# Performance work log

Hardware: AMD Instinct MI355X
Metric: run time of the kernel (lower is better)

The kernel has to match this reference:

```python
import jax, jax.numpy as jnp
import numpy as np

NEG_INF = -jnp.inf


def apply_top_k_top_p(logits, k, p):
    """Faithful port of vllm apply_top_k_top_p (both k and p given).
    logits: [B, V] float; k: [B] int (1..V); p: [B] float in (0,1].
    """
    B, V = logits.shape
    # ascending sort, as in torch logits.sort(descending=False)
    idx = jnp.argsort(logits, axis=-1)                      # [B, V]
    ls = jnp.take_along_axis(logits, idx, axis=-1)          # [B, V] sorted ascending
    # ---- top-k: threshold = k-th largest = sorted[V - k] ----
    thr_idx = (V - k.astype(jnp.int32))[:, None]            # [B, 1]
    thr = jnp.take_along_axis(ls, thr_idx, axis=-1)         # [B, 1]
    ls = jnp.where(ls < thr, NEG_INF, ls)
    # ---- top-p: mask smallest tail whose cumulative prob <= 1 - p ----
    probs_sort = jax.nn.softmax(ls, axis=-1)
    probs_sum = jnp.cumsum(probs_sort, axis=-1)
    top_p_mask = probs_sum <= (1.0 - p)[:, None]
    # last (largest) element is never masked
    col = jnp.arange(V)
    top_p_mask = top_p_mask & (col[None, :] != V - 1)
    ls = jnp.where(top_p_mask, NEG_INF, ls)
    # ---- scatter back to original positions ----
    rows = jnp.arange(B)[:, None]
    return jnp.zeros_like(logits).at[rows, idx].set(ls)


def setup_inputs() -> dict:
    key = jax.random.key(0)
    k1, k2, k3, k4 = jax.random.split(key, 4)
    B, V = 256, 128000
    logits = jax.random.normal(k1, (B, V), dtype=jnp.float32) * 4.0
    k = jax.random.randint(k2, (B,), 1, V + 1, dtype=jnp.int32)
    p = jax.random.uniform(k3, (B,), dtype=jnp.float32, minval=0.05, maxval=1.0)
    # Exp(1) noise, replacing torch q.exponential_() in random_sample
    q = jax.random.exponential(k4, (B, V), dtype=jnp.float32)
    return {"logits": logits, "k": k, "p": p, "q": q}


def reference(logits, k, p, q):
    masked = apply_top_k_top_p(logits, k, p)
    # logprobs_mode == 'processed_logprobs'
    logprobs = jax.nn.log_softmax(masked.astype(jnp.float32), axis=-1)
    probs = jax.nn.softmax(masked.astype(jnp.float32), axis=-1)
    # random_sample: argmax(probs / Exp(1) noise) == Gumbel-max style sampling
    next_token_ids = jnp.argmax(probs / q, axis=-1).reshape(-1)
    return next_token_ids, logprobs
```

## Files before the change

kernel.cpp:

```cpp
#include <hip/hip_runtime.h>
#include <stdint.h>
#include <math.h>

#define TPB 1024
#define NWAVE 16
#define NBINS 8192
#define CAP 4096
#define TIE_CAP 4096
#define NEG_SENTINEL -1.0e30f

struct Scal {
  double Eacc, T, T2, Zall, D, Zf, logZf, Wtmp, Wb1b, cumexcl;
  float M;
  int b1, bw, m;
  unsigned int trank, sel, ccur, cnt_tmp;
  unsigned int n1, n2, cnt_v, ntie, cnt_b1;
};

__device__ __forceinline__ unsigned int f2key(float x) {
  unsigned int b = __float_as_uint(x);
  return (b & 0x80000000u) ? ~b : (b | 0x80000000u);
}
__device__ __forceinline__ float key2f(unsigned int u) {
  unsigned int b = (u & 0x80000000u) ? (u ^ 0x80000000u) : ~u;
  return __uint_as_float(b);
}

__global__ __launch_bounds__(TPB, 1) void topk_topp_kernel(
    const float* __restrict__ logits, const int* __restrict__ kk,
    const float* __restrict__ pp, const float* __restrict__ qq,
    float* __restrict__ out, int B, int V)
{
  __shared__ __align__(16) char smem[123392];
  double* w_hist = (double*)smem;
  double* col_w  = (double*)smem;
  unsigned int* cnt_hist = (unsigned int*)(smem + 65536);
  unsigned int* col_key  = (unsigned int*)(smem + 65536);
  unsigned int* col_idx  = (unsigned int*)(smem + 81920);
  unsigned int* b1_keys  = (unsigned int*)(smem + 98304);
  unsigned int* tie_idx  = (unsigned int*)(smem + 98304);
  double* dscan = (double*)(smem + 114688);
  unsigned int* uscan = (unsigned int*)(smem + 114688);
  float* fscan = (float*)(smem + 114688);
  Scal* S = (Scal*)(smem + 122880);

  const int row = blockIdx.x;
  const int tid = threadIdx.x;
  const size_t roff = (size_t)row * (size_t)V;
  const float* L = logits + roff;
  const float* Q = qq + roff;
  float* OLP = out + B + roff;
  const int V4 = V >> 2;
  const float4* L4 = (const float4*)L;
  const float4* Q4 = (const float4*)Q;

  for (int i = tid; i < NBINS; i += TPB) cnt_hist[i] = 0u;
  if (tid == 0) { S->n1 = 0u; S->n2 = 0u; S->cnt_v = 0u; S->ntie = 0u; S->bw = -1; }
  __syncthreads();

  float lmax = -INFINITY;
  for (int j = tid; j < V4; j += TPB) {
    float4 v = L4[j];
    lmax = fmaxf(lmax, fmaxf(fmaxf(v.x, v.y), fmaxf(v.z, v.w)));
    atomicAdd(&cnt_hist[f2key(v.x) >> 19], 1u);
    atomicAdd(&cnt_hist[f2key(v.y) >> 19], 1u);
    atomicAdd(&cnt_hist[f2key(v.z) >> 19], 1u);
    atomicAdd(&cnt_hist[f2key(v.w) >> 19], 1u);
  }
  for (int i = (V4 << 2) + tid; i < V; i += TPB) {
    float x = L[i]; lmax = fmaxf(lmax, x);
    atomicAdd(&cnt_hist[f2key(x) >> 19], 1u);
  }
  #pragma unroll
  for (int o = 32; o; o >>= 1) lmax = fmaxf(lmax, __shfl_down(lmax, o, 64));
  if ((tid & 63) == 0) fscan[tid >> 6] = lmax;
  __syncthreads();
  if (tid == 0) {
    float m = fscan[0];
    for (int i = 1; i < NWAVE; ++i) m = fmaxf(m, fscan[i]);
    S->M = m;
  }
  __syncthreads();
  const float Mf = S->M;
  const double Md = (double)Mf;

  {
    int kv = kk[row]; if (kv < 1) kv = 1; if (kv > V) kv = V;
    unsigned int target = (unsigned int)(V - kv);
    const int per = NBINS / TPB;
    const int base = tid * per;
    unsigned int own = 0;
    for (int b = 0; b < per; ++b) own += cnt_hist[base + b];
    uscan[tid] = own;
    __syncthreads();
    for (int off = 1; off < TPB; off <<= 1) {
      unsigned int v = uscan[tid];
      unsigned int a = (tid >= off) ? uscan[tid - off] : 0u;
      __syncthreads();
      uscan[tid] = v + a;
      __syncthreads();
    }
    unsigned int cum = uscan[tid] - own;
    for (int b = 0; b < per; ++b) {
      unsigned int c = cnt_hist[base + b];
      if (target >= cum && target < cum + c) {
        S->b1 = base + b; S->trank = target - cum; S->cnt_b1 = c;
      }
      cum += c;
    }
  }
  __syncthreads();
  const int b1 = S->b1;
  const unsigned int cnt_b1 = S->cnt_b1;
  const bool fast1 = (cnt_b1 <= (unsigned int)CAP);

  for (int i = tid; i < NBINS; i += TPB) w_hist[i] = 0.0;
  __syncthreads();
  for (int j = tid; j < V4; j += TPB) {
    float4 v = L4[j];
    float xs[4] = {v.x, v.y, v.z, v.w};
    #pragma unroll
    for (int c = 0; c < 4; ++c) {
      float x = xs[c];
      unsigned int u = f2key(x);
      double e = exp((double)x - Md);
      unsafeAtomicAdd(&w_hist[u >> 19], e);
      if (fast1 && (int)(u >> 19) == b1) {
        unsigned int ppos = atomicAdd(&S->n1, 1u);
        if (ppos < (unsigned int)CAP) b1_keys[ppos] = u;
      }
    }
  }
  for (int i = (V4 << 2) + tid; i < V; i += TPB) {
    float x = L[i];
    unsigned int u = f2key(x);
    double e = exp((double)x - Md);
    unsafeAtomicAdd(&w_hist[u >> 19], e);
    if (fast1 && (int)(u >> 19) == b1) {
      unsigned int ppos = atomicAdd(&S->n1, 1u);
      if (ppos < (unsigned int)CAP) b1_keys[ppos] = u;
    }
  }
  __syncthreads();

  unsigned int thr_key = 0u;
  {
    unsigned int prefix = (unsigned int)b1;
    int plen = 13;
    unsigned int trank = S->trank;
    unsigned int ccur = cnt_b1;
    bool have = fast1;
    while (!have && ccur > (unsigned int)CAP && plen < 32) {
      int nb = 32 - plen; if (nb > 13) nb = 13;
      int nbins = 1 << nb;
      for (int i = tid; i < nbins; i += TPB) cnt_hist[i] = 0u;
      __syncthreads();
      const int shp = 32 - plen, shs = 32 - plen - nb;
      for (int i2 = tid; i2 < V; i2 += TPB) {
        unsigned int u = f2key(L[i2]);
        if ((u >> shp) == prefix) atomicAdd(&cnt_hist[(u >> shs) & (unsigned int)(nbins - 1)], 1u);
      }
      __syncthreads();
      if (tid == 0) {
        unsigned int cum = 0;
        for (int c = 0; c < nbins; ++c) {
          unsigned int cc = cnt_hist[c];
          if (trank >= cum && trank < cum + cc) { S->sel = (unsigned int)c; S->trank = trank - cum; S->ccur = cc; break; }
          cum += cc;
        }
      }
      __syncthreads();
      prefix = (prefix << nb) | S->sel;
      trank = S->trank;
      ccur = S->ccur;
      plen += nb;
    }
    if (!have && ccur <= (unsigned int)CAP) {
      if (tid == 0) S->n1 = 0u;
      __syncthreads();
      const int shp = 32 - plen;
      for (int i2 = tid; i2 < V; i2 += TPB) {
        unsigned int u = f2key(L[i2]);
        if ((u >> shp) == prefix) { unsigned int ppos = atomicAdd(&S->n1, 1u); if (ppos < (unsigned int)CAP) b1_keys[ppos] = u; }
      }
      __syncthreads();
      have = true;
    }
    if (!have) {
      thr_key = prefix;
    } else {
      unsigned int n1e = S->n1; if (n1e > (unsigned int)CAP) n1e = CAP;
      unsigned int lo = prefix << (32 - plen);
      for (int bit = 32 - plen - 1; bit >= 0; --bit) {
        unsigned int mid = lo | (1u << bit);
        unsigned int lc = 0;
        for (unsigned int i2 = tid; i2 < n1e; i2 += TPB) {
          unsigned int u = b1_keys[i2];
          lc += (u >= lo && u < mid) ? 1u : 0u;
        }
        #pragma unroll
        for (int o = 32; o; o >>= 1) lc += __shfl_down(lc, o, 64);
        if ((tid & 63) == 0) uscan[tid >> 6] = lc;
        __syncthreads();
        if (tid == 0) { unsigned int s = 0; for (int i3 = 0; i3 < NWAVE; ++i3) s += uscan[i3]; S->cnt_tmp = s; }
        __syncthreads();
        unsigned int c = S->cnt_tmp;
        if (trank >= c) { trank -= c; lo = mid; }
        __syncthreads();
      }
      thr_key = lo;
    }
  }

  {
    double wl = 0.0;
    if (fast1) {
      unsigned int n1e = S->n1; if (n1e > (unsigned int)CAP) n1e = CAP;
      for (unsigned int i2 = tid; i2 < n1e; i2 += TPB) {
        unsigned int u = b1_keys[i2];
        if (u < thr_key) wl += exp((double)key2f(u) - Md);
      }
    } else {
      for (int i2 = tid; i2 < V; i2 += TPB) {
        float x = L[i2];
        unsigned int u = f2key(x);
        if ((int)(u >> 19) == b1 && u < thr_key) wl += exp((double)x - Md);
      }
    }
    #pragma unroll
    for (int o = 32; o; o >>= 1) wl += __shfl_down(wl, o, 64);
    if ((tid & 63) == 0) dscan[tid >> 6] = wl;
    __syncthreads();
    if (tid == 0) { double s = 0; for (int i3 = 0; i3 < NWAVE; ++i3) s += dscan[i3]; S->Wb1b = s; }
    __syncthreads();
  }
  {
    double za = 0.0, zb = 0.0;
    for (int i = tid; i < NBINS; i += TPB) {
      double w = w_hist[i];
      za += w; if (i < b1) zb += w;
    }
    #pragma unroll
    for (int o = 32; o; o >>= 1) { za += __shfl_down(za, o, 64); zb += __shfl_down(zb, o, 64); }
    if ((tid & 63) == 0) { dscan[tid >> 6] = za; dscan[NWAVE + (tid >> 6)] = zb; }
    __syncthreads();
    if (tid == 0) {
      double sza = 0, szb = 0;
      for (int i3 = 0; i3 < NWAVE; ++i3) { sza += dscan[i3]; szb += dscan[NWAVE + i3]; }
      double D = szb + S->Wb1b;
      S->Zall = sza; S->D = D;
      float pv = pp[row];
      float omp = 1.0f - pv;
      double T = (double)omp * (sza - D);
      S->T = T; S->T2 = T + D;
    }
    __syncthreads();
  }
  {
    const double T2 = S->T2;
    const int per = NBINS / TPB;
    const int base = tid * per;
    double own = 0.0;
    for (int b = 0; b < per; ++b) own += w_hist[base + b];
    dscan[tid] = own;
    __syncthreads();
    for (int off = 1; off < TPB; off <<= 1) {
      double v = dscan[tid];
      double a = (tid >= off) ? dscan[tid - off] : 0.0;
      __syncthreads();
      dscan[tid] = v + a;
      __syncthreads();
    }
    double cum = dscan[tid] - own;
    for (int b = 0; b < per; ++b) {
      double w = w_hist[base + b];
      if (T2 >= cum && T2 < cum + w) { S->bw = base + b; S->cumexcl = cum; }
      cum += w;
    }
    __syncthreads();
    if (tid == 0) {
      if (S->bw < 0) {
        for (int bq = NBINS - 1; bq >= 0; --bq)
          if (w_hist[bq] > 0.0) { S->bw = bq; S->cumexcl = S->Zall - w_hist[bq]; break; }
      }
      double ea = S->cumexcl - S->D;
      S->Eacc = ea > 0.0 ? ea : 0.0;
    }
    __syncthreads();
  }

  unsigned int vstar = 0u; double E_before = 0.0;
  {
    int plen2 = 13;
    unsigned int prefix2 = (unsigned int)S->bw;
    bool direct = false;
    while (true) {
      if (tid == 0) S->n2 = 0u;
      __syncthreads();
      const int shp = 32 - plen2;
      for (int j = tid; j < V4; j += TPB) {
        float4 v = L4[j];
        const int i0 = j << 2;
        float xs[4] = {v.x, v.y, v.z, v.w};
        #pragma unroll
        for (int c = 0; c < 4; ++c) {
          float x = xs[c];
          unsigned int u = f2key(x);
          if (u >= thr_key && (u >> shp) == prefix2) {
            unsigned int ppos = atomicAdd(&S->n2, 1u);
            if (ppos < (unsigned int)CAP) { col_key[ppos] = u; col_idx[ppos] = (unsigned int)(i0 + c); col_w[ppos] = exp((double)x - Md); }
          }
        }
      }
      for (int i2 = (V4 << 2) + tid; i2 < V; i2 += TPB) {
        float x = L[i2]; unsigned int u = f2key(x);
        if (u >= thr_key && (u >> shp) == prefix2) {
          unsigned int ppos = atomicAdd(&S->n2, 1u);
          if (ppos < (unsigned int)CAP) { col_key[ppos] = u; col_idx[ppos] = (unsigned int)i2; col_w[ppos] = exp((double)x - Md); }
        }
      }
      __syncthreads();
      if (S->n2 <= (unsigned int)CAP) break;
      if (plen2 >= 32) { direct = true; break; }
      int nb = 32 - plen2; if (nb > 13) nb = 13;
      int nbins = 1 << nb;
      for (int i = tid; i < nbins; i += TPB) w_hist[i] = 0.0;
      __syncthreads();
      const int shs = 32 - plen2 - nb;
      for (int i2 = tid; i2 < V; i2 += TPB) {
        float x = L[i2]; unsigned int u = f2key(x);
        if (u >= thr_key && (u >> shp) == prefix2)
          unsafeAtomicAdd(&w_hist[(u >> shs) & (unsigned int)(nbins - 1)], exp((double)x - Md));
      }
      __syncthreads();
      if (tid == 0) {
        double Trem = S->T - S->Eacc;
        double cum = 0.0; int csel = -1; double cumsel = 0.0;
        for (int c = 0; c < nbins; ++c) {
          double w = w_hist[c];
          if (Trem >= cum && Trem < cum + w) { csel = c; cumsel = cum; break; }
          cum += w;
        }
        if (csel < 0) {
          cum = 0.0;
          for (int c = 0; c < nbins; ++c) { double w = w_hist[c]; if (w > 0.0) { csel = c; cumsel = cum; } cum += w; }
        }
        S->sel = (unsigned int)csel;
        S->Eacc += cumsel;
      }
      __syncthreads();
      prefix2 = (prefix2 << nb) | S->sel;
      plen2 += nb;
    }

    if (direct) {
      vstar = prefix2; E_before = S->Eacc;
      unsigned int n2e = S->n2; if (n2e > (unsigned int)CAP) n2e = CAP;
      if (n2e > (unsigned int)TIE_CAP) n2e = TIE_CAP;
      for (unsigned int i2 = tid; i2 < n2e; i2 += TPB) tie_idx[i2] = col_idx[i2];
      if (tid == 0) { S->cnt_v = S->n2; S->ntie = n2e; }
      __syncthreads();
    } else {
      unsigned int n2e = S->n2; if (n2e > (unsigned int)CAP) n2e = CAP;
      unsigned int lo = prefix2 << (32 - plen2);
      double Ea = S->Eacc;
      const double T = S->T;
      for (int bit = 32 - plen2 - 1; bit >= 0; --bit) {
        unsigned int mid = lo | (1u << bit);
        double lw = 0.0;
        for (unsigned int i2 = tid; i2 < n2e; i2 += TPB) {
          unsigned int u = col_key[i2];
          if (u >= lo && u < mid) lw += col_w[i2];
        }
        #pragma unroll
        for (int o = 32; o; o >>= 1) lw += __shfl_down(lw, o, 64);
        if ((tid & 63) == 0) dscan[tid >> 6] = lw;
        __syncthreads();
        if (tid == 0) { double s = 0; for (int i3 = 0; i3 < NWAVE; ++i3) s += dscan[i3]; S->Wtmp = s; }
        __syncthreads();
        double W = S->Wtmp;
        if (Ea + W > T) {  } else { Ea += W; lo = mid; }
        __syncthreads();
      }
      vstar = lo; E_before = Ea;
      for (unsigned int i2 = tid; i2 < n2e; i2 += TPB) {
        if (col_key[i2] == vstar) {
          atomicAdd(&S->cnt_v, 1u);
          unsigned int tp = atomicAdd(&S->ntie, 1u);
          if (tp < (unsigned int)TIE_CAP) tie_idx[tp] = col_idx[i2];
        }
      }
      __syncthreads();
    }
  }

  if (tid == 0) {
    double e_v = exp((double)key2f(vstar) - Md);
    double md = floor((S->T - E_before) / e_v);
    double cv = (double)S->cnt_v;
    if (!(md > 0.0)) md = 0.0;
    if (md > cv) md = cv;
    S->m = (int)md;
    double Zk = S->Zall - S->D;
    double Zf = Zk - (E_before + md * e_v);
    if (!(Zf > 1e-300)) Zf = 1e-300;
    S->Zf = Zf; S->logZf = log(Zf);
  }
  __syncthreads();

  const unsigned int vs = vstar;
  const int mth = S->m;
  int nt = (int)S->ntie; if (nt > TIE_CAP) nt = TIE_CAP;
  const float Zff = (float)S->Zf;
  const double lZf = S->logZf;
  float br = -1.0f; int bi = 0x7FFFFFFF;

  for (int j = tid; j < V4; j += TPB) {
    float4 lv = L4[j];
    float4 qv = Q4[j];
    const int i0 = j << 2;
    float xs[4] = {lv.x, lv.y, lv.z, lv.w};
    float qs[4] = {qv.x, qv.y, qv.z, qv.w};
    #pragma unroll
    for (int c = 0; c < 4; ++c) {
      const int i = i0 + c;
      float x = xs[c];
      unsigned int u = f2key(x);
      bool keep;
      if (u > vs) keep = true;
      else if (u == vs) {
        int rk = 0;
        for (int t2 = 0; t2 < nt; ++t2) rk += (tie_idx[t2] < (unsigned int)i) ? 1 : 0;
        keep = (rk >= mth);
      } else keep = false;
      float lp, r;
      if (keep) {
        lp = (float)(((double)x - Md) - lZf);
        float pr = expf(x - Mf) / Zff;
        r = pr / qs[c];
      } else { lp = NEG_SENTINEL; r = 0.0f; }
      OLP[i] = lp;
      if (r > br || (r == br && i < bi)) { br = r; bi = i; }
    }
  }
  for (int i = (V4 << 2) + tid; i < V; i += TPB) {
    float x = L[i];
    unsigned int u = f2key(x);
    bool keep;
    if (u > vs) keep = true;
    else if (u == vs) {
      int rk = 0;
      for (int t2 = 0; t2 < nt; ++t2) rk += (tie_idx[t2] < (unsigned int)i) ? 1 : 0;
      keep = (rk >= mth);
    } else keep = false;
    float lp, r;
    if (keep) {
      lp = (float)(((double)x - Md) - lZf);
      float pr = expf(x - Mf) / Zff;
      r = pr / Q[i];
    } else { lp = NEG_SENTINEL; r = 0.0f; }
    OLP[i] = lp;
    if (r > br || (r == br && i < bi)) { br = r; bi = i; }
  }

  #pragma unroll
  for (int o = 32; o; o >>= 1) {
    float orr = __shfl_down(br, o, 64);
    int oi = __shfl_down(bi, o, 64);
    if (orr > br || (orr == br && oi < bi)) { br = orr; bi = oi; }
  }
  __syncthreads();
  if ((tid & 63) == 0) { fscan[tid >> 6] = br; ((int*)(fscan + NWAVE))[tid >> 6] = bi; }
  __syncthreads();
  if (tid == 0) {
    float bb = fscan[0]; int bbi = ((int*)(fscan + NWAVE))[0];
    for (int i = 1; i < NWAVE; ++i) {
      float r2 = fscan[i]; int ii = ((int*)(fscan + NWAVE))[i];
      if (r2 > bb || (r2 == bb && ii < bbi)) { bb = r2; bbi = ii; }
    }
    out[row] = (float)bbi;
  }
}

extern "C" void kernel_launch(void* const* d_in, const int* in_sizes, int n_in,
                              void* d_out, int out_size, void* d_ws, size_t ws_size,
                              hipStream_t stream) {
  const float* logits = (const float*)d_in[0];
  const int* k = (const int*)d_in[1];
  const float* p = (const float*)d_in[2];
  const float* q = (const float*)d_in[3];
  float* out = (float*)d_out;
  const int B = in_sizes[1];
  const int V = in_sizes[0] / B;
  hipLaunchKernelGGL(topk_topp_kernel, dim3(B), dim3(TPB), 0, stream,
                     logits, k, p, q, out, B, V);
}
```

Baseline: 454.7 us.

## Fuse weight histogram into first pass and replace bit-by-bit radix refinement

```diff
diff --git a/kernel.cpp b/kernel.cpp
--- a/kernel.cpp
+++ b/kernel.cpp
@@ -10,10 +10,10 @@
 #define NEG_SENTINEL -1.0e30f
 
 struct Scal {
-  double Eacc, T, T2, Zall, D, Zf, logZf, Wtmp, Wb1b, cumexcl;
+  double Eacc, T, T2, Zall, D, Zf, logZf, Wb1b, cumexcl;
   float M;
   int b1, bw, m;
-  unsigned int trank, sel, ccur, cnt_tmp;
+  unsigned int trank, sel, ccur;
   unsigned int n1, n2, cnt_v, ntie, cnt_b1;
 };
 
@@ -31,7 +31,7 @@
     const float* __restrict__ pp, const float* __restrict__ qq,
     float* __restrict__ out, int B, int V)
 {
-  __shared__ __align__(16) char smem[123392];
+  __shared__ __align__(16) char smem[118400];
   double* w_hist = (double*)smem;
   double* col_w  = (double*)smem;
   unsigned int* cnt_hist = (unsigned int*)(smem + 65536);
@@ -39,13 +39,18 @@
   unsigned int* col_idx  = (unsigned int*)(smem + 81920);
   unsigned int* b1_keys  = (unsigned int*)(smem + 98304);
   unsigned int* tie_idx  = (unsigned int*)(smem + 98304);
-  double* dscan = (double*)(smem + 114688);
-  unsigned int* uscan = (unsigned int*)(smem + 114688);
-  float* fscan = (float*)(smem + 114688);
-  Scal* S = (Scal*)(smem + 122880);
+  unsigned int* rcnt = (unsigned int*)(smem + 114688);
+  double*       rw   = (double*)(smem + 115712);
+  double*       dw   = (double*)(smem + 117760);
+  unsigned int* uw   = (unsigned int*)(smem + 118016);
+  float*        fw   = (float*)(smem + 118080);
+  int*          iw   = (int*)(smem + 118144);
+  Scal* S = (Scal*)(smem + 118208);
 
   const int row = blockIdx.x;
   const int tid = threadIdx.x;
+  const int lane = tid & 63;
+  const int wid = tid >> 6;
   const size_t roff = (size_t)row * (size_t)V;
   const float* L = logits + roff;
   const float* Q = qq + roff;
@@ -54,105 +59,119 @@
   const float4* L4 = (const float4*)L;
   const float4* Q4 = (const float4*)Q;
 
-  for (int i = tid; i < NBINS; i += TPB) cnt_hist[i] = 0u;
+  for (int i = tid; i < NBINS; i += TPB) { cnt_hist[i] = 0u; w_hist[i] = 0.0; }
   if (tid == 0) { S->n1 = 0u; S->n2 = 0u; S->cnt_v = 0u; S->ntie = 0u; S->bw = -1; }
   __syncthreads();
 
   float lmax = -INFINITY;
   for (int j = tid; j < V4; j += TPB) {
     float4 v = L4[j];
-    lmax = fmaxf(lmax, fmaxf(fmaxf(v.x, v.y), fmaxf(v.z, v.w)));
-    atomicAdd(&cnt_hist[f2key(v.x) >> 19], 1u);
-    atomicAdd(&cnt_hist[f2key(v.y) >> 19], 1u);
-    atomicAdd(&cnt_hist[f2key(v.z) >> 19], 1u);
-    atomicAdd(&cnt_hist[f2key(v.w) >> 19], 1u);
+    float xs[4] = {v.x, v.y, v.z, v.w};
+    #pragma unroll
+    for (int c = 0; c < 4; ++c) {
+      float x = xs[c];
+      lmax = fmaxf(lmax, x);
+      unsigned int u = f2key(x);
+      atomicAdd(&cnt_hist[u >> 19], 1u);
+      float bl = key2f(u & 0xFFF80000u);
+      unsafeAtomicAdd(&w_hist[u >> 19], (double)__expf(x - bl));
+    }
   }
   for (int i = (V4 << 2) + tid; i < V; i += TPB) {
-    float x = L[i]; lmax = fmaxf(lmax, x);
-    atomicAdd(&cnt_hist[f2key(x) >> 19], 1u);
+    float x = L[i];
+    lmax = fmaxf(lmax, x);
+    unsigned int u = f2key(x);
+    atomicAdd(&cnt_hist[u >> 19], 1u);
+    float bl = key2f(u & 0xFFF80000u);
+    unsafeAtomicAdd(&w_hist[u >> 19], (double)__expf(x - bl));
   }
   #pragma unroll
   for (int o = 32; o; o >>= 1) lmax = fmaxf(lmax, __shfl_down(lmax, o, 64));
-  if ((tid & 63) == 0) fscan[tid >> 6] = lmax;
+  if (lane == 0) fw[wid] = lmax;
   __syncthreads();
   if (tid == 0) {
-    float m = fscan[0];
-    for (int i = 1; i < NWAVE; ++i) m = fmaxf(m, fscan[i]);
+    float m = fw[0];
+    for (int i = 1; i < NWAVE; ++i) m = fmaxf(m, fw[i]);
     S->M = m;
   }
   __syncthreads();
   const float Mf = S->M;
   const double Md = (double)Mf;
 
+  for (int i = tid; i < NBINS; i += TPB) {
+    double w = w_hist[i];
+    if (w != 0.0) {
+      float bl = key2f(((unsigned int)i) << 19);
+      w_hist[i] = w * exp((double)bl - Md);
+    }
+  }
+  __syncthreads();
+
   {
     int kv = kk[row]; if (kv < 1) kv = 1; if (kv > V) kv = V;
-    unsigned int target = (unsigned int)(V - kv);
-    const int per = NBINS / TPB;
-    const int base = tid * per;
+    const unsigned int target = (unsigned int)(V - kv);
+    const int base = tid * 8;
     unsigned int own = 0;
-    for (int b = 0; b < per; ++b) own += cnt_hist[base + b];
-    uscan[tid] = own;
-    __syncthreads();
-    for (int off = 1; off < TPB; off <<= 1) {
-      unsigned int v = uscan[tid];
-      unsigned int a = (tid >= off) ? uscan[tid - off] : 0u;
-      __syncthreads();
-      uscan[tid] = v + a;
-      __syncthreads();
-    }
-    unsigned int cum = uscan[tid] - own;
-    for (int b = 0; b < per; ++b) {
+    #pragma unroll
+    for (int b = 0; b < 8; ++b) own += cnt_hist[base + b];
+    unsigned int inc = own;
+    #pragma unroll
+    for (int o = 1; o < 64; o <<= 1) {
+      unsigned int t = __shfl_up(inc, (unsigned)o, 64);
+      if (lane >= o) inc += t;
+    }
+    if (lane == 63) uw[wid] = inc;
+    __syncthreads();
+    if (tid == 0) {
+      unsigned int c = 0;
+      for (int w = 0; w < NWAVE; ++w) { unsigned int t = uw[w]; uw[w] = c; c += t; }
+    }
+    __syncthreads();
+    unsigned int cum = uw[wid] + (inc - own);
+    for (int b = 0; b < 8; ++b) {
       unsigned int c = cnt_hist[base + b];
-      if (target >= cum && target < cum + c) {
+      if (c && target >= cum && target < cum + c) {
         S->b1 = base + b; S->trank = target - cum; S->cnt_b1 = c;
       }
       cum += c;
     }
   }
   __syncthreads();
+
   const int b1 = S->b1;
   const unsigned int cnt_b1 = S->cnt_b1;
   const bool fast1 = (cnt_b1 <= (unsigned int)CAP);
-
-  for (int i = tid; i < NBINS; i += TPB) w_hist[i] = 0.0;
-  __syncthreads();
-  for (int j = tid; j < V4; j += TPB) {
-    float4 v = L4[j];
-    float xs[4] = {v.x, v.y, v.z, v.w};
-    #pragma unroll
-    for (int c = 0; c < 4; ++c) {
-      float x = xs[c];
-      unsigned int u = f2key(x);
-      double e = exp((double)x - Md);
-      unsafeAtomicAdd(&w_hist[u >> 19], e);
-      if (fast1 && (int)(u >> 19) == b1) {
-        unsigned int ppos = atomicAdd(&S->n1, 1u);
-        if (ppos < (unsigned int)CAP) b1_keys[ppos] = u;
-      }
-    }
-  }
-  for (int i = (V4 << 2) + tid; i < V; i += TPB) {
-    float x = L[i];
-    unsigned int u = f2key(x);
-    double e = exp((double)x - Md);
-    unsafeAtomicAdd(&w_hist[u >> 19], e);
-    if (fast1 && (int)(u >> 19) == b1) {
-      unsigned int ppos = atomicAdd(&S->n1, 1u);
-      if (ppos < (unsigned int)CAP) b1_keys[ppos] = u;
-    }
-  }
-  __syncthreads();
-
-  unsigned int thr_key = 0u;
-  {
-    unsigned int prefix = (unsigned int)b1;
-    int plen = 13;
-    unsigned int trank = S->trank;
+  const float bl1 = key2f(((unsigned int)b1) << 19);
+  const double fac1 = exp((double)bl1 - Md);
+
+  unsigned int prefix = (unsigned int)b1;
+  int plen = 13;
+  if (fast1) {
+    for (int j = tid; j < V4; j += TPB) {
+      float4 v = L4[j];
+      float xs[4] = {v.x, v.y, v.z, v.w};
+      #pragma unroll
+      for (int c = 0; c < 4; ++c) {
+        unsigned int u = f2key(xs[c]);
+        if ((int)(u >> 19) == b1) {
+          unsigned int pos = atomicAdd(&S->n1, 1u);
+          if (pos < (unsigned int)CAP) b1_keys[pos] = u;
+        }
+      }
+    }
+    for (int i = (V4 << 2) + tid; i < V; i += TPB) {
+      unsigned int u = f2key(L[i]);
+      if ((int)(u >> 19) == b1) {
+        unsigned int pos = atomicAdd(&S->n1, 1u);
+        if (pos < (unsigned int)CAP) b1_keys[pos] = u;
+      }
+    }
+    __syncthreads();
+  } else {
     unsigned int ccur = cnt_b1;
-    bool have = fast1;
-    while (!have && ccur > (unsigned int)CAP && plen < 32) {
+    while (ccur > (unsigned int)CAP && plen < 32) {
       int nb = 32 - plen; if (nb > 13) nb = 13;
-      int nbins = 1 << nb;
+      const int nbins = 1 << nb;
       for (int i = tid; i < nbins; i += TPB) cnt_hist[i] = 0u;
       __syncthreads();
       const int shp = 32 - plen, shs = 32 - plen - nb;
@@ -162,76 +181,85 @@
       }
       __syncthreads();
       if (tid == 0) {
-        unsigned int cum = 0;
+        unsigned int trank = S->trank, cum = 0;
         for (int c = 0; c < nbins; ++c) {
           unsigned int cc = cnt_hist[c];
-          if (trank >= cum && trank < cum + cc) { S->sel = (unsigned int)c; S->trank = trank - cum; S->ccur = cc; break; }
+          if (cc && trank < cum + cc) { S->sel = (unsigned int)c; S->trank = trank - cum; S->ccur = cc; break; }
           cum += cc;
         }
       }
       __syncthreads();
       prefix = (prefix << nb) | S->sel;
-      trank = S->trank;
       ccur = S->ccur;
       plen += nb;
     }
-    if (!have && ccur <= (unsigned int)CAP) {
-      if (tid == 0) S->n1 = 0u;
-      __syncthreads();
-      const int shp = 32 - plen;
-      for (int i2 = tid; i2 < V; i2 += TPB) {
-        unsigned int u = f2key(L[i2]);
-        if ((u >> shp) == prefix) { unsigned int ppos = atomicAdd(&S->n1, 1u); if (ppos < (unsigned int)CAP) b1_keys[ppos] = u; }
-      }
-      __syncthreads();
-      have = true;
-    }
-    if (!have) {
-      thr_key = prefix;
-    } else {
-      unsigned int n1e = S->n1; if (n1e > (unsigned int)CAP) n1e = CAP;
-      unsigned int lo = prefix << (32 - plen);
-      for (int bit = 32 - plen - 1; bit >= 0; --bit) {
-        unsigned int mid = lo | (1u << bit);
-        unsigned int lc = 0;
-        for (unsigned int i2 = tid; i2 < n1e; i2 += TPB) {
-          unsigned int u = b1_keys[i2];
-          lc += (u >= lo && u < mid) ? 1u : 0u;
-        }
-        #pragma unroll
-        for (int o = 32; o; o >>= 1) lc += __shfl_down(lc, o, 64);
-        if ((tid & 63) == 0) uscan[tid >> 6] = lc;
-        __syncthreads();
-        if (tid == 0) { unsigned int s = 0; for (int i3 = 0; i3 < NWAVE; ++i3) s += uscan[i3]; S->cnt_tmp = s; }
-        __syncthreads();
-        unsigned int c = S->cnt_tmp;
-        if (trank >= c) { trank -= c; lo = mid; }
-        __syncthreads();
-      }
-      thr_key = lo;
-    }
-  }
+    if (tid == 0) S->n1 = 0u;
+    __syncthreads();
+    const int shp = 32 - plen;
+    for (int i2 = tid; i2 < V; i2 += TPB) {
+      unsigned int u = f2key(L[i2]);
+      if ((u >> shp) == prefix) {
+        unsigned int pos = atomicAdd(&S->n1, 1u);
+        if (pos < (unsigned int)CAP) b1_keys[pos] = u;
+      }
+    }
+    __syncthreads();
+  }
+
+  {
+    const unsigned int n1e = (S->n1 < (unsigned int)CAP) ? S->n1 : (unsigned int)CAP;
+    while (plen < 32) {
+      int nb = 32 - plen; if (nb > 8) nb = 8;
+      const int shp = 32 - plen, shs = 32 - plen - nb;
+      const unsigned int msk = (1u << nb) - 1u;
+      if (tid < 256) rcnt[tid] = 0u;
+      __syncthreads();
+      for (unsigned int i = tid; i < n1e; i += TPB) {
+        unsigned int u = b1_keys[i];
+        if ((u >> shp) == prefix) atomicAdd(&rcnt[(u >> shs) & msk], 1u);
+      }
+      __syncthreads();
+      if (tid == 0) {
+        unsigned int trank = S->trank, cum = 0; int sel = -1;
+        const int nbn = 1 << nb;
+        for (int c = 0; c < nbn; ++c) {
+          unsigned int cc = rcnt[c];
+          if (cc && trank < cum + cc) { sel = c; S->trank = trank - cum; break; }
+          cum += cc;
+        }
+        if (sel < 0) {
+          for (int c = nbn - 1; c >= 0; --c) if (rcnt[c]) { sel = c; S->trank = rcnt[c] - 1u; break; }
+          if (sel < 0) sel = 0;
+        }
+        S->sel = (unsigned int)sel;
+      }
+      __syncthreads();
+      prefix = (prefix << nb) | S->sel;
+      plen += nb;
+    }
+  }
+  const unsigned int thr_key = prefix;
 
   {
     double wl = 0.0;
     if (fast1) {
-      unsigned int n1e = S->n1; if (n1e > (unsigned int)CAP) n1e = CAP;
-      for (unsigned int i2 = tid; i2 < n1e; i2 += TPB) {
-        unsigned int u = b1_keys[i2];
-        if (u < thr_key) wl += exp((double)key2f(u) - Md);
+      const unsigned int n1e = (S->n1 < (unsigned int)CAP) ? S->n1 : (unsigned int)CAP;
+      for (unsigned int i = tid; i < n1e; i += TPB) {
+        unsigned int u = b1_keys[i];
+        if (u < thr_key) wl += (double)__expf(key2f(u) - bl1);
       }
     } else {
       for (int i2 = tid; i2 < V; i2 += TPB) {
         float x = L[i2];
         unsigned int u = f2key(x);
-        if ((int)(u >> 19) == b1 && u < thr_key) wl += exp((double)x - Md);
+        if ((int)(u >> 19) == b1 && u < thr_key) wl += (double)__expf(x - bl1);
       }
     }
     #pragma unroll
     for (int o = 32; o; o >>= 1) wl += __shfl_down(wl, o, 64);
-    if ((tid & 63) == 0) dscan[tid >> 6] = wl;
-    __syncthreads();
-    if (tid == 0) { double s = 0; for (int i3 = 0; i3 < NWAVE; ++i3) s += dscan[i3]; S->Wb1b = s; }
+    if (lane == 0) dw[wid] = wl;
+    __syncthreads();
+    if (tid == 0) { double s = 0; for (int i = 0; i < NWAVE; ++i) s += dw[i]; S->Wb1b = s * fac1; }
     __syncthreads();
   }
   {
@@ -242,11 +270,11 @@
     }
     #pragma unroll
     for (int o = 32; o; o >>= 1) { za += __shfl_down(za, o, 64); zb += __shfl_down(zb, o, 64); }
-    if ((tid & 63) == 0) { dscan[tid >> 6] = za; dscan[NWAVE + (tid >> 6)] = zb; }
+    if (lane == 0) { dw[wid] = za; dw[NWAVE + wid] = zb; }
     __syncthreads();
     if (tid == 0) {
       double sza = 0, szb = 0;
-      for (int i3 = 0; i3 < NWAVE; ++i3) { sza += dscan[i3]; szb += dscan[NWAVE + i3]; }
+      for (int i = 0; i < NWAVE; ++i) { sza += dw[i]; szb += dw[NWAVE + i]; }
       double D = szb + S->Wb1b;
       S->Zall = sza; S->D = D;
       float pv = pp[row];
@@ -256,25 +284,30 @@
     }
     __syncthreads();
   }
+
   {
     const double T2 = S->T2;
-    const int per = NBINS / TPB;
-    const int base = tid * per;
+    const int base = tid * 8;
     double own = 0.0;
-    for (int b = 0; b < per; ++b) own += w_hist[base + b];
-    dscan[tid] = own;
-    __syncthreads();
-    for (int off = 1; off < TPB; off <<= 1) {
-      double v = dscan[tid];
-      double a = (tid >= off) ? dscan[tid - off] : 0.0;
-      __syncthreads();
-      dscan[tid] = v + a;
-      __syncthreads();
-    }
-    double cum = dscan[tid] - own;
-    for (int b = 0; b < per; ++b) {
+    #pragma unroll
+    for (int b = 0; b < 8; ++b) own += w_hist[base + b];
+    double incd = own;
+    #pragma unroll
+    for (int o = 1; o < 64; o <<= 1) {
+      double t = __shfl_up(incd, (unsigned)o, 64);
+      if (lane >= o) incd += t;
+    }
+    if (lane == 63) dw[wid] = incd;
+    __syncthreads();
+    if (tid == 0) {
+      double c = 0;
+      for (int w = 0; w < NWAVE; ++w) { double t = dw[w]; dw[w] = c; c += t; }
+    }
+    __syncthreads();
+    double cum = dw[wid] + (incd - own);
+    for (int b = 0; b < 8; ++b) {
       double w = w_hist[base + b];
-      if (T2 >= cum && T2 < cum + w) { S->bw = base + b; S->cumexcl = cum; }
+      if (w > 0.0 && T2 >= cum && T2 < cum + w) { S->bw = base + b; S->cumexcl = cum; }
       cum += w;
     }
     __syncthreads();
@@ -291,8 +324,11 @@
 
   unsigned int vstar = 0u; double E_before = 0.0;
   {
+    const int bwv = S->bw;
+    const float blw = key2f(((unsigned int)bwv) << 19);
+    const double facw = exp((double)blw - Md);
     int plen2 = 13;
-    unsigned int prefix2 = (unsigned int)S->bw;
+    unsigned int prefix2 = (unsigned int)bwv;
     bool direct = false;
     while (true) {
       if (tid == 0) S->n2 = 0u;
@@ -307,45 +343,54 @@
           float x = xs[c];
           unsigned int u = f2key(x);
           if (u >= thr_key && (u >> shp) == prefix2) {
-            unsigned int ppos = atomicAdd(&S->n2, 1u);
-            if (ppos < (unsigned int)CAP) { col_key[ppos] = u; col_idx[ppos] = (unsigned int)(i0 + c); col_w[ppos] = exp((double)x - Md); }
+            unsigned int pos = atomicAdd(&S->n2, 1u);
+            if (pos < (unsigned int)CAP) {
+              col_key[pos] = u; col_idx[pos] = (unsigned int)(i0 + c);
+              col_w[pos] = (double)__expf(x - blw) * facw;
+            }
           }
         }
       }
       for (int i2 = (V4 << 2) + tid; i2 < V; i2 += TPB) {
-        float x = L[i2]; unsigned int u = f2key(x);
+        float x = L[i2];
+        unsigned int u = f2key(x);
         if (u >= thr_key && (u >> shp) == prefix2) {
-          unsigned int ppos = atomicAdd(&S->n2, 1u);
-          if (ppos < (unsigned int)CAP) { col_key[ppos] = u; col_idx[ppos] = (unsigned int)i2; col_w[ppos] = exp((double)x - Md); }
+          unsigned int pos = atomicAdd(&S->n2, 1u);
+          if (pos < (unsigned int)CAP) {
+            col_key[pos] = u; col_idx[pos] = (unsigned int)i2;
+            col_w[pos] = (double)__expf(x - blw) * facw;
+          }
         }
       }
       __syncthreads();
       if (S->n2 <= (unsigned int)CAP) break;
       if (plen2 >= 32) { direct = true; break; }
       int nb = 32 - plen2; if (nb > 13) nb = 13;
-      int nbins = 1 << nb;
+      const int nbins = 1 << nb;
       for (int i = tid; i < nbins; i += TPB) w_hist[i] = 0.0;
       __syncthreads();
       const int shs = 32 - plen2 - nb;
       for (int i2 = tid; i2 < V; i2 += TPB) {
-        float x = L[i2]; unsigned int u = f2key(x);
+        float x = L[i2];
+        unsigned int u = f2key(x);
         if (u >= thr_key && (u >> shp) == prefix2)
-          unsafeAtomicAdd(&w_hist[(u >> shs) & (unsigned int)(nbins - 1)], exp((double)x - Md));
+          unsafeAtomicAdd(&w_hist[(u >> shs) & (unsigned int)(nbins - 1)], (double)__expf(x - blw) * facw);
       }
       __syncthreads();
       if (tid == 0) {
         double Trem = S->T - S->Eacc;
-        double cum = 0.0; int csel = -1; double cumsel = 0.0;
+        double cum = 0.0; int sel = -1; double cumsel = 0.0;
         for (int c = 0; c < nbins; ++c) {
           double w = w_hist[c];
-          if (Trem >= cum && Trem < cum + w) { csel = c; cumsel = cum; break; }
+          if (w > 0.0 && cum + w > Trem) { sel = c; cumsel = cum; break; }
           cum += w;
         }
-        if (csel < 0) {
+        if (sel < 0) {
           cum = 0.0;
-          for (int c = 0; c < nbins; ++c) { double w = w_hist[c]; if (w > 0.0) { csel = c; cumsel = cum; } cum += w; }
-        }
-        S->sel = (unsigned int)csel;
+          for (int c = 0; c < nbins; ++c) { double w = w_hist[c]; if (w > 0.0) { sel = c; cumsel = cum; } cum += w; }
+        }
+        if (sel < 0) sel = 0;
+        S->sel = (unsigned int)sel;
         S->Eacc += cumsel;
       }
       __syncthreads();
@@ -357,56 +402,68 @@
       vstar = prefix2; E_before = S->Eacc;
       unsigned int n2e = S->n2; if (n2e > (unsigned int)CAP) n2e = CAP;
       if (n2e > (unsigned int)TIE_CAP) n2e = TIE_CAP;
-      for (unsigned int i2 = tid; i2 < n2e; i2 += TPB) tie_idx[i2] = col_idx[i2];
+      for (unsigned int i = tid; i < n2e; i += TPB) tie_idx[i] = col_idx[i];
       if (tid == 0) { S->cnt_v = S->n2; S->ntie = n2e; }
       __syncthreads();
     } else {
-      unsigned int n2e = S->n2; if (n2e > (unsigned int)CAP) n2e = CAP;
-      unsigned int lo = prefix2 << (32 - plen2);
-      double Ea = S->Eacc;
-      const double T = S->T;
-      for (int bit = 32 - plen2 - 1; bit >= 0; --bit) {
-        unsigned int mid = lo | (1u << bit);
-        double lw = 0.0;
-        for (unsigned int i2 = tid; i2 < n2e; i2 += TPB) {
-          unsigned int u = col_key[i2];
-          if (u >= lo && u < mid) lw += col_w[i2];
-        }
-        #pragma unroll
-        for (int o = 32; o; o >>= 1) lw += __shfl_down(lw, o, 64);
-        if ((tid & 63) == 0) dscan[tid >> 6] = lw;
+      const unsigned int n2e = (S->n2 < (unsigned int)CAP) ? S->n2 : (unsigned int)CAP;
+      while (plen2 < 32) {
+        int nb = 32 - plen2; if (nb > 8) nb = 8;
+        const int shp = 32 - plen2, shs = 32 - plen2 - nb;
+        const unsigned int msk = (1u << nb) - 1u;
+        if (tid < 256) rw[tid] = 0.0;
         __syncthreads();
-        if (tid == 0) { double s = 0; for (int i3 = 0; i3 < NWAVE; ++i3) s += dscan[i3]; S->Wtmp = s; }
+        for (unsigned int i = tid; i < n2e; i += TPB) {
+          unsigned int u = col_key[i];
+          if ((u >> shp) == prefix2) unsafeAtomicAdd(&rw[(u >> shs) & msk], col_w[i]);
+        }
         __syncthreads();
-        double W = S->Wtmp;
-        if (Ea + W > T) {  } else { Ea += W; lo = mid; }
+        if (tid == 0) {
+          double Trem = S->T - S->Eacc;
+          double cum = 0.0; int sel = -1; double cumsel = 0.0;
+          const int nbn = 1 << nb;
+          for (int c = 0; c < nbn; ++c) {
+            double w = rw[c];
+            if (w > 0.0 && cum + w > Trem) { sel = c; cumsel = cum; break; }
+            cum += w;
+          }
+          if (sel < 0) {
+            cum = 0.0;
+            for (int c = 0; c < nbn; ++c) { double w = rw[c]; if (w > 0.0) { sel = c; cumsel = cum; } cum += w; }
+          }
+          if (sel < 0) sel = 0;
+          S->sel = (unsigned int)sel;
+          S->Eacc += cumsel;
+        }
         __syncthreads();
-      }
-      vstar = lo; E_before = Ea;
-      for (unsigned int i2 = tid; i2 < n2e; i2 += TPB) {
-        if (col_key[i2] == vstar) {
+        prefix2 = (prefix2 << nb) | S->sel;
+        plen2 += nb;
+      }
+      vstar = prefix2; E_before = S->Eacc;
+      for (unsigned int i = tid; i < n2e; i += TPB) {
+        if (col_key[i] == vstar) {
           atomicAdd(&S->cnt_v, 1u);
           unsigned int tp = atomicAdd(&S->ntie, 1u);
-          if (tp < (unsigned int)TIE_CAP) tie_idx[tp] = col_idx[i2];
-        }
-      }
-      __syncthreads();
-    }
-  }
-
-  if (tid == 0) {
-    double e_v = exp((double)key2f(vstar) - Md);
-    double md = floor((S->T - E_before) / e_v);
-    double cv = (double)S->cnt_v;
-    if (!(md > 0.0)) md = 0.0;
-    if (md > cv) md = cv;
-    S->m = (int)md;
-    double Zk = S->Zall - S->D;
-    double Zf = Zk - (E_before + md * e_v);
-    if (!(Zf > 1e-300)) Zf = 1e-300;
-    S->Zf = Zf; S->logZf = log(Zf);
-  }
-  __syncthreads();
+          if (tp < (unsigned int)TIE_CAP) tie_idx[tp] = col_idx[i];
+        }
+      }
+      __syncthreads();
+    }
+
+    if (tid == 0) {
+      double e_v = (double)__expf(key2f(vstar) - blw) * facw;
+      double md = floor((S->T - E_before) / e_v);
+      double cv = (double)S->cnt_v;
+      if (!(md > 0.0)) md = 0.0;
+      if (md > cv) md = cv;
+      S->m = (int)md;
+      double Zk = S->Zall - S->D;
+      double Zf = Zk - (E_before + md * e_v);
+      if (!(Zf > 1e-300)) Zf = 1e-300;
+      S->Zf = Zf; S->logZf = log(Zf);
+    }
+    __syncthreads();
+  }
 
   const unsigned int vs = vstar;
   const int mth = S->m;
@@ -470,12 +527,12 @@
     if (orr > br || (orr == br && oi < bi)) { br = orr; bi = oi; }
   }
   __syncthreads();
-  if ((tid & 63) == 0) { fscan[tid >> 6] = br; ((int*)(fscan + NWAVE))[tid >> 6] = bi; }
+  if (lane == 0) { fw[wid] = br; iw[wid] = bi; }
   __syncthreads();
   if (tid == 0) {
-    float bb = fscan[0]; int bbi = ((int*)(fscan + NWAVE))[0];
+    float bb = fw[0]; int bbi = iw[0];
     for (int i = 1; i < NWAVE; ++i) {
-      float r2 = fscan[i]; int ii = ((int*)(fscan + NWAVE))[i];
+      float r2 = fw[i]; int ii = iw[i];
       if (r2 > bb || (r2 == bb && ii < bbi)) { bb = r2; bbi = ii; }
     }
     out[row] = (float)bbi;
```

New measurement: 446.6 us. Within noise of the previous version (-1.8%).
